# Performance work log

Measured on AMD Instinct MI355X. Metric: run time of the kernel, lower is better.

The kernel has to match this reference:

```python
import jax, jax.numpy as jnp
import numpy as np
from jax import lax

D_MODEL = 512
INPUT_DIM = 64
D_INNER = 1024      # expand * d_model
D_STATE = 128
NHEADS = 16         # d_inner // headdim (headdim = ssm_state//num_heads = 64)
HEADDIM = 64
D_CONV = 4
CONV_DIM = D_INNER + 2 * D_STATE          # 1280 (ngroups=1)
D_IN_PROJ = 2 * D_INNER + 2 * D_STATE + NHEADS  # 2320
BATCH = 2
SEQ = 1024
MASK_RATIO = 0.75
EPS = 1e-5


def setup_inputs() -> dict:
    key = jax.random.key(0)
    ks = jax.random.split(key, 14)
    s = lambda fan: 1.0 / np.sqrt(fan)
    return {
        "x": jax.random.normal(ks[0], (BATCH, SEQ, INPUT_DIM), jnp.float32),
        "conv_emb_w": jax.random.normal(ks[1], (D_MODEL, INPUT_DIM, 3), jnp.float32) * s(INPUT_DIM * 3),
        "conv_emb_b": jax.random.normal(ks[2], (D_MODEL,), jnp.float32) * 0.02,
        "cls_token": jax.random.normal(ks[3], (1, 1, D_MODEL), jnp.float32) * 0.02,
        "in_proj_w": jax.random.normal(ks[4], (D_IN_PROJ, D_MODEL), jnp.float32) * s(D_MODEL),
        "conv1d_w": jax.random.normal(ks[5], (CONV_DIM, 1, D_CONV), jnp.float32) * s(D_CONV),
        "conv1d_b": jax.random.normal(ks[6], (CONV_DIM,), jnp.float32) * 0.02,
        "dt_bias": jax.random.uniform(ks[7], (NHEADS,), jnp.float32, -4.0, 0.0),
        "A_log": jnp.log(jax.random.uniform(ks[8], (NHEADS,), jnp.float32, 1.0, 16.0)),
        "D": jax.random.normal(ks[9], (NHEADS,), jnp.float32),
        "rms_w": jnp.ones((D_INNER,), jnp.float32),
        "out_proj_w": jax.random.normal(ks[10], (D_MODEL, D_INNER), jnp.float32) * s(D_INNER),
        "ln_g": jnp.ones((D_MODEL,), jnp.float32),
        "ln_b": jnp.zeros((D_MODEL,), jnp.float32),
    }


def _forward(x, conv_emb_w, conv_emb_b, cls_token, in_proj_w, conv1d_w, conv1d_b,
             dt_bias, A_log, D, rms_w, out_proj_w, ln_g, ln_b):
    b = x.shape[0]
    # ---- conv embedding: Conv1d(k=3, pad=1) over time ----
    xe = lax.conv_general_dilated(x.transpose(0, 2, 1), conv_emb_w, (1,), [(1, 1)],
                                  dimension_numbers=("NCH", "OIH", "NCH"))
    xe = (xe + conv_emb_b[None, :, None]).transpose(0, 2, 1)  # (b, L, d_model)
    # ---- append CLS token at end ----
    h = jnp.concatenate([xe, jnp.broadcast_to(cls_token, (b, 1, D_MODEL))], axis=1)
    L = h.shape[1]
    # ---- Mamba2 block ----
    zxbcdt = jnp.einsum("bld,ed->ble", h, in_proj_w)  # (b, L, 2320)
    z = zxbcdt[..., :D_INNER]
    xBC = zxbcdt[..., D_INNER:D_INNER + CONV_DIM]
    dt = jax.nn.softplus(zxbcdt[..., -NHEADS:] + dt_bias)  # (b, L, h)
    # causal depthwise conv (pad left d_conv-1) + SiLU
    xBC = lax.conv_general_dilated(xBC.transpose(0, 2, 1), conv1d_w, (1,), [(D_CONV - 1, 0)],
                                   dimension_numbers=("NCH", "OIH", "NCH"),
                                   feature_group_count=CONV_DIM)
    xBC = jax.nn.silu((xBC + conv1d_b[None, :, None]).transpose(0, 2, 1))  # (b, L, 1280)
    x_in = xBC[..., :D_INNER].reshape(b, L, NHEADS, HEADDIM)   # (b, L, h, p)
    B = xBC[..., D_INNER:D_INNER + D_STATE]                     # (b, L, n)
    C = xBC[..., D_INNER + D_STATE:]                            # (b, L, n)
    A = -jnp.exp(A_log)                                         # (h,)
    dA = jnp.exp(dt * A)                                        # (b, L, h)
    # selective state-space scan; state (b, h, p, n)
    def step(state, inp):
        x_t, dt_t, B_t, C_t, dA_t = inp  # (b,h,p) (b,h) (b,n) (b,n) (b,h)
        state = state * dA_t[:, :, None, None] + \
            (dt_t[:, :, None] * x_t)[..., None] * B_t[:, None, None, :]
        y_t = jnp.einsum("bhpn,bn->bhp", state, C_t)
        return state, y_t
    s0 = jnp.zeros((b, NHEADS, HEADDIM, D_STATE), x.dtype)
    _, ys = lax.scan(step, s0, (x_in.transpose(1, 0, 2, 3), dt.transpose(1, 0, 2),
                                B.transpose(1, 0, 2), C.transpose(1, 0, 2),
                                dA.transpose(1, 0, 2)))
    y = ys.transpose(1, 0, 2, 3) + D[None, None, :, None] * x_in  # (b, L, h, p)
    y = y.reshape(b, L, D_INNER)
    # gated RMSNorm: gate first, then normalize
    y = y * jax.nn.silu(z)
    y = y * lax.rsqrt(jnp.mean(y * y, axis=-1, keepdims=True) + EPS) * rms_w
    out = jnp.einsum("ble,de->bld", y, out_proj_w)  # (b, L, d_model)
    # ---- LayerNorm ----
    mu = jnp.mean(out, axis=-1, keepdims=True)
    var = jnp.mean((out - mu) ** 2, axis=-1, keepdims=True)
    out = (out - mu) * lax.rsqrt(var + EPS) * ln_g + ln_b
    return out


def reference(x, conv_emb_w, conv_emb_b, cls_token, in_proj_w, conv1d_w, conv1d_b,
              dt_bias, A_log, D, rms_w, out_proj_w, ln_g, ln_b):
    out = _forward(x, conv_emb_w, conv_emb_b, cls_token, in_proj_w, conv1d_w, conv1d_b,
                   dt_bias, A_log, D, rms_w, out_proj_w, ln_g, ln_b)
    b = out.shape[0]
    cls = out[:, -1:, :]
    body = out[:, :-1, :]                      # (b, SEQ, d)
    len_keep = int(SEQ * (1 - MASK_RATIO))     # 256
    noise = jax.random.uniform(jax.random.fold_in(jax.random.key(0), 1), (b, SEQ))
    ids_shuffle = jnp.argsort(noise, axis=1)
    ids_restore = jnp.argsort(ids_shuffle, axis=1)
    ids_keep = ids_shuffle[:, :len_keep]
    x_masked = jnp.take_along_axis(body, ids_keep[:, :, None], axis=1)
    mask = jnp.where(jnp.arange(SEQ)[None, :] < len_keep, 0.0, 1.0)
    mask = jnp.take_along_axis(jnp.broadcast_to(mask, (b, SEQ)), ids_restore, axis=1)
    x_out = jnp.concatenate([x_masked, cls], axis=1)  # (b, len_keep+1, d)
    return (x_out, mask, ids_restore, ids_keep)
```

## Files before the change

### kernel.cpp

```cpp
#include <hip/hip_runtime.h>
#include <hip/hip_bf16.h>
#include <stdint.h>

#define LTOK  1025
#define NROWS 2050
#define DM    512
#define DIN   1024
#define DST   128
#define NHEAD 16
#define HDIM  64
#define CDIM  1280
#define EPROJ 2320
#define QC    64
#define NCH   17

#define O_RIDX   0
#define O_CB     1024
#define O_CLS    1536
#define O_C1B    2048
#define O_DTB    3328
#define O_ALOG   3344
#define O_DV     3360
#define O_RMSW   3376
#define O_LNG    4400
#define O_LNB    4912
#define O_CW     5440
#define O_IPW    103744
#define O_OPW    1291584
#define O_C1W    1815872
#define O_CX     1820992
#define O_ZX     1952064
#define O_XBC    6708064
#define O_DT     9332064
#define O_LGA    9364864
#define O_Y      9397664
#define O_H      9397664
#define O_X3     10447264
#define O_OUTG   11496864
#define O_SL     11760032
#define O_CLA    16216480
#define O_SL2    16251296
#define O_KEEP   18479520

#define OO_MASK 263168
#define OO_IDR  265216
#define OO_IDK  267264

typedef __attribute__((ext_vector_type(8))) short short8;
typedef __attribute__((ext_vector_type(4))) short shortx4;
typedef __attribute__((ext_vector_type(4))) float floatx4;

__device__ __forceinline__ short f2bs(float f) {
  union { float f; uint32_t u; } v; v.f = f;
  uint32_t r = (v.u + 0x7FFFu + ((v.u >> 16) & 1u)) >> 16;
  return (short)r;
}
__device__ __forceinline__ float bf2f(uint16_t u) {
  return __uint_as_float(((uint32_t)u) << 16);
}

struct InPtrs { const void* p[14]; };

__device__ __forceinline__ uint32_t rotl32(uint32_t v, int d) {
  return (v << d) | (v >> (32 - d));
}
__device__ void threefry2x32(uint32_t k0, uint32_t k1, uint32_t c0, uint32_t c1,
                             uint32_t& o0, uint32_t& o1) {
  uint32_t ks0 = k0, ks1 = k1, ks2 = 0x1BD11BDAu ^ k0 ^ k1;
  uint32_t x0 = c0 + ks0, x1 = c1 + ks1;
#define TF_R4(a,b,c,d) \
  x0 += x1; x1 = rotl32(x1,a); x1 ^= x0; \
  x0 += x1; x1 = rotl32(x1,b); x1 ^= x0; \
  x0 += x1; x1 = rotl32(x1,c); x1 ^= x0; \
  x0 += x1; x1 = rotl32(x1,d); x1 ^= x0;
  TF_R4(13,15,26,6)  x0 += ks1; x1 += ks2 + 1u;
  TF_R4(17,29,16,24) x0 += ks2; x1 += ks0 + 2u;
  TF_R4(13,15,26,6)  x0 += ks0; x1 += ks1 + 3u;
  TF_R4(17,29,16,24) x0 += ks1; x1 += ks2 + 4u;
  TF_R4(13,15,26,6)  x0 += ks2; x1 += ks0 + 5u;
#undef TF_R4
  o0 = x0; o1 = x1;
}

__device__ int detect_is_f32(const uint32_t* w, int nelem) {
  int nw = nelem / 2; if (nw > 16) nw = 16;
  int insane = 0, lozero = 0, anynz = 0;
  for (int i = 0; i < nw; ++i) {
    uint32_t word = w[i];
    if (word != 0u) anynz = 1;
    uint32_t lo = word & 0xffffu;
    if (lo == 0u) { lozero++; continue; }
    float v = __uint_as_float(lo << 16);
    float a = fabsf(v);
    if (!(a >= 1e-8f && a <= 1e4f)) insane++;
  }
  if (insane >= 2) return 1;
  if (lozero == nw && anynz) return 1;
  return 0;
}

__global__ __launch_bounds__(256) void k_convert(InPtrs ptrs, float* ws,
                                                 float* out, int* rowidx) {
  static const int sizes[13] = {98304, 512, 512, 1187840, 5120, 1280,
                                16, 16, 16, 1024, 524288, 512, 512};
  static const int offs[13]  = {O_CW, O_CB, O_CLS, O_IPW, O_C1W, O_C1B,
                                O_DTB, O_ALOG, O_DV, O_RMSW, O_OPW, O_LNG, O_LNB};
  static const int isbf[13]  = {1,0,0,1,0,0,0,0,0,0,1,0,0};
  int t = blockIdx.y;
  int tid = threadIdx.x;

  if (t >= 14) {
    int b = t - 14;
    int idx = blockIdx.x;
    if (idx > 1024) return;
    if (idx == 1024) {
      const uint32_t* cp = (const uint32_t*)ptrs.p[3];
      __shared__ int cf;
      if (tid == 0) cf = detect_is_f32(cp, 512);
      __syncthreads();
      uint16_t* hout = (uint16_t*)(ws + O_H);
      for (int cch = tid; cch < DM; cch += 256) {
        float v = cf ? ((const float*)cp)[cch] : bf2f(((const uint16_t*)cp)[cch]);
        hout[((long)(b * LTOK + 1024)) * DM + cch] = (uint16_t)f2bs(v);
      }
      return;
    }
    const uint32_t* xp = (const uint32_t*)ptrs.p[0];
    __shared__ int xf;
    if (tid == 0) xf = detect_is_f32(xp, 131072);
    __syncthreads();
    if (tid < 192) {
      int i = tid / 3, k = tid % 3;
      int tt = idx + k - 1;
      float v = 0.f;
      if (tt >= 0 && tt < 1024) {
        long src = ((long)(b * 1024 + tt)) * 64 + i;
        v = xf ? ((const float*)xp)[src] : bf2f(((const uint16_t*)xp)[src]);
      }
      ((uint16_t*)(ws + O_X3))[((long)(b * 1024 + idx)) * 192 + tid] = (uint16_t)f2bs(v);
    }
    return;
  }

  if (t == 13) {
    int bx = blockIdx.x;
    if (bx < 257) {
      int base = (bx * 256 + tid) * 4;
      if (base < 263168)
        *(float4*)(ws + O_OUTG + base) = make_float4(0.f, 0.f, 0.f, 0.f);
      return;
    }
    if (bx < 512 || bx >= 544) return;
    int rb = bx - 512;
    int seg = rb & 15, b = rb >> 4;
    uint8_t* keep = (uint8_t*)(ws + O_KEEP);
    __shared__ float vals[1024];
    uint32_t fk0, fk1;
    threefry2x32(0u, 0u, 0u, 1u, fk0, fk1);
#pragma unroll
    for (int k = 0; k < 4; ++k) {
      int i = tid + k * 256;
      uint32_t o0, o1;
      threefry2x32(fk0, fk1, 0u, (uint32_t)(b * 1024 + i), o0, o1);
      uint32_t bits = o0 ^ o1;
      vals[i] = __uint_as_float((bits >> 9) | 0x3f800000u) - 1.0f;
    }
    __syncthreads();
    int tg = seg * 64 + (tid >> 2);
    int qq = tid & 3;
    float v = vals[tg];
    int r = 0;
    int j0 = qq * 256;
    for (int it = 0; it < 256; ++it) {
      int j = j0 + ((it + qq * 8) & 255);
      float vj = vals[j];
      r += (vj < v || (vj == v && j < tg)) ? 1 : 0;
    }
    r += __shfl_xor(r, 1, 64);
    r += __shfl_xor(r, 2, 64);
    if (qq == 0) {
      out[OO_IDR + b * 1024 + tg] = (float)r;
      out[OO_MASK + b * 1024 + tg] = (r < 256) ? 0.0f : 1.0f;
      keep[b * LTOK + tg] = (r < 256) ? 1 : 0;
      if (r < 256) {
        out[OO_IDK + b * 256 + r] = (float)tg;
        rowidx[b * 257 + r] = b * LTOK + tg;
      }
      if (tg == 0) {
        rowidx[b * 257 + 256] = b * LTOK + 1024;
        keep[b * LTOK + 1024] = 1;
      }
    }
    return;
  }

  int n = sizes[t];
  const uint32_t* w = (const uint32_t*)ptrs.p[t + 1];
  __shared__ int sf;
  if (tid == 0) sf = detect_is_f32(w, n);
  __syncthreads();
  int base = (blockIdx.x * 256 + tid) * 4;
  if (base >= n) return;
  if (isbf[t]) {
    ushort4 o;
    if (sf) {
      const float4 vv = *(const float4*)((const float*)w + base);
      o.x = (uint16_t)f2bs(vv.x); o.y = (uint16_t)f2bs(vv.y);
      o.z = (uint16_t)f2bs(vv.z); o.w = (uint16_t)f2bs(vv.w);
    } else {
      const uint32_t* s = w + (base >> 1);
      uint32_t w0 = s[0], w1 = s[1];
      o.x = (uint16_t)(w0 & 0xffffu); o.y = (uint16_t)(w0 >> 16);
      o.z = (uint16_t)(w1 & 0xffffu); o.w = (uint16_t)(w1 >> 16);
    }
    *(ushort4*)((uint16_t*)(ws + offs[t]) + base) = o;
  } else {
    float* dst = ws + offs[t];
    if (sf) {
      *(float4*)(dst + base) = *(const float4*)((const float*)w + base);
    } else {
      const uint32_t* s = w + (base >> 1);
      uint32_t w0 = s[0], w1 = s[1];
      float4 o;
      o.x = __uint_as_float((w0 & 0xffffu) << 16);
      o.y = __uint_as_float(w0 & 0xffff0000u);
      o.z = __uint_as_float((w1 & 0xffffu) << 16);
      o.w = __uint_as_float(w1 & 0xffff0000u);
      *(float4*)(dst + base) = o;
    }
  }
}

__global__ __launch_bounds__(256) void k_bgemm(
    const void* __restrict__ A, const uint16_t* __restrict__ Bw,
    void* __restrict__ C, const float* __restrict__ bias,
    const int* __restrict__ rowmap, int M, int N, int K, int ldc,
    int cmode, int abf, int obf) {
  __shared__ __align__(16) short sA[2][128 * 40];
  __shared__ __align__(16) short sB[2][128 * 40];
  int tid = threadIdx.x;
  int lane = tid & 63, w = tid >> 6;
  int lm = lane & 15, q = lane >> 4;
  int wm = (w >> 1) * 64, wn = (w & 1) * 64;
  int bm = blockIdx.y * 128, bn = blockIdx.x * 128;
  int gz = gridDim.z;
  int Ks = K / gz;
  int kbase = blockIdx.z * Ks;
  int nk = Ks >> 5;

  int srow[4], scol[4];
  long aoff[4]; bool aok[4]; long boff[4]; bool bok[4];
#pragma unroll
  for (int it = 0; it < 4; ++it) {
    int e4 = (tid + it * 256) * 4;
    srow[it] = e4 >> 5; scol[it] = e4 & 31;
    int gm = bm + srow[it];
    aok[it] = gm < M;
    aoff[it] = aok[it] ? (long)(rowmap ? rowmap[gm] : gm) * K : 0;
    int gn = bn + srow[it];
    bok[it] = gn < N;
    boff[it] = bok[it] ? (long)gn * K : 0;
  }

  auto gload = [&](int kt, float4* vaf, ushort4* vau, ushort4* vb) {
    int kc = kbase + kt * 32;
#pragma unroll
    for (int it = 0; it < 4; ++it) {
      if (abf) {
        if (aok[it]) vau[it] = *(const ushort4*)((const uint16_t*)A + aoff[it] + kc + scol[it]);
        else { vau[it].x = 0; vau[it].y = 0; vau[it].z = 0; vau[it].w = 0; }
      } else {
        vaf[it] = aok[it] ? *(const float4*)((const float*)A + aoff[it] + kc + scol[it])
                          : make_float4(0.f, 0.f, 0.f, 0.f);
      }
      if (bok[it]) vb[it] = *(const ushort4*)(Bw + boff[it] + kc + scol[it]);
      else { vb[it].x = 0; vb[it].y = 0; vb[it].z = 0; vb[it].w = 0; }
    }
  };
  auto sstore = [&](int buf, const float4* vaf, const ushort4* vau, const ushort4* vb) {
#pragma unroll
    for (int it = 0; it < 4; ++it) {
      if (abf)
        *(ushort4*)&sA[buf][srow[it] * 40 + scol[it]] = vau[it];
      else
        *(shortx4*)&sA[buf][srow[it] * 40 + scol[it]] =
            shortx4{f2bs(vaf[it].x), f2bs(vaf[it].y), f2bs(vaf[it].z), f2bs(vaf[it].w)};
      *(ushort4*)&sB[buf][srow[it] * 40 + scol[it]] = vb[it];
    }
  };

  floatx4 acc[4][4] = {};
  float4 vaf[4], naf[4];
  ushort4 vau[4], nau[4], vb[4], nb[4];

  gload(0, vaf, vau, vb);
  sstore(0, vaf, vau, vb);
  for (int kt = 0; kt < nk; ++kt) {
    int cur = kt & 1;
    if (kt + 1 < nk) gload(kt + 1, naf, nau, nb);
    __syncthreads();
    short8 afrag[4], bfrag[4];
#pragma unroll
    for (int i = 0; i < 4; ++i)
      afrag[i] = *(const short8*)&sA[cur][(wm + i * 16 + lm) * 40 + q * 8];
#pragma unroll
    for (int j = 0; j < 4; ++j)
      bfrag[j] = *(const short8*)&sB[cur][(wn + j * 16 + lm) * 40 + q * 8];
#pragma unroll
    for (int i = 0; i < 4; ++i)
#pragma unroll
      for (int j = 0; j < 4; ++j)
        acc[i][j] = __builtin_amdgcn_mfma_f32_16x16x32_bf16(afrag[i], bfrag[j], acc[i][j], 0, 0, 0);
    if (kt + 1 < nk) sstore(1 - cur, naf, nau, nb);
  }

#pragma unroll
  for (int i = 0; i < 4; ++i) {
    int rowl = wm + i * 16 + q * 4;
#pragma unroll
    for (int reg = 0; reg < 4; ++reg) {
      int r = bm + rowl + reg;
      if (r >= M) continue;
      long crow = cmode ? (long)((r >> 10) * LTOK + (r & 1023)) : (long)r;
#pragma unroll
      for (int j = 0; j < 4; ++j) {
        int ccol = bn + wn + j * 16 + lm;
        if (ccol < N) {
          float v = acc[i][j][reg];
          if (gz > 1) {
            atomicAdd(&((float*)C)[crow * ldc + ccol], v);
          } else {
            if (bias) v += bias[ccol];
            if (obf) ((uint16_t*)C)[crow * ldc + ccol] = (uint16_t)f2bs(v);
            else ((float*)C)[crow * ldc + ccol] = v;
          }
        }
      }
    }
  }
}

__global__ __launch_bounds__(256) void k_conv1d(const uint16_t* __restrict__ zx,
                                                const float* __restrict__ w,
                                                const float* __restrict__ bias,
                                                uint16_t* __restrict__ xbc,
                                                const float* __restrict__ dtb,
                                                const float* __restrict__ alog,
                                                float* __restrict__ dt,
                                                float* __restrict__ lga) {
  long rp_ = blockIdx.x;
  if (rp_ >= NROWS) {
    int idx = (int)(rp_ - NROWS) * 256 + threadIdx.x;
    if (idx < NROWS * NHEAD) {
      int rr = idx >> 4, h = idx & 15;
      float xv = bf2f(zx[(long)rr * EPROJ + (EPROJ - NHEAD) + h]) + dtb[h];
      float dtv = (xv > 20.f) ? xv : log1pf(expf(xv));
      dt[idx] = dtv;
      lga[idx] = dtv * (-expf(alog[h]));
    }
    return;
  }
  {
    int xcd = (int)(rp_ & 7), slot = (int)(rp_ >> 3);
    rp_ = (xcd < 2) ? (long)xcd * 257 + slot
                    : (long)514 + (long)(xcd - 2) * 256 + slot;
  }
  long r = rp_;
  int b = (int)(r / LTOK), t = (int)(r % LTOK);
  for (int c4 = threadIdx.x * 4; c4 < CDIM; c4 += 1024) {
    float4 bi = *(const float4*)(bias + c4);
    float a0 = bi.x, a1 = bi.y, a2 = bi.z, a3 = bi.w;
    float4 w0 = *(const float4*)(w + (c4 + 0) * 4);
    float4 w1 = *(const float4*)(w + (c4 + 1) * 4);
    float4 w2 = *(const float4*)(w + (c4 + 2) * 4);
    float4 w3 = *(const float4*)(w + (c4 + 3) * 4);
    float wr0[4] = {w0.x, w0.y, w0.z, w0.w};
    float wr1[4] = {w1.x, w1.y, w1.z, w1.w};
    float wr2[4] = {w2.x, w2.y, w2.z, w2.w};
    float wr3[4] = {w3.x, w3.y, w3.z, w3.w};
#pragma unroll
    for (int k = 0; k < 4; ++k) {
      int tt = t - 3 + k;
      if (tt >= 0) {
        ushort4 xv = *(const ushort4*)(zx + ((long)(b * LTOK + tt)) * EPROJ + DIN + c4);
        a0 = fmaf(wr0[k], bf2f(xv.x), a0);
        a1 = fmaf(wr1[k], bf2f(xv.y), a1);
        a2 = fmaf(wr2[k], bf2f(xv.z), a2);
        a3 = fmaf(wr3[k], bf2f(xv.w), a3);
      }
    }
    ushort4 o;
    o.x = (uint16_t)f2bs(a0 / (1.f + expf(-a0)));
    o.y = (uint16_t)f2bs(a1 / (1.f + expf(-a1)));
    o.z = (uint16_t)f2bs(a2 / (1.f + expf(-a2)));
    o.w = (uint16_t)f2bs(a3 / (1.f + expf(-a3)));
    *(ushort4*)(xbc + r * CDIM + c4) = o;
  }
}

__global__ __launch_bounds__(256) void k_ssd1(const uint16_t* __restrict__ xbc,
                                              const float* __restrict__ dt,
                                              const float* __restrict__ lga,
                                              float* __restrict__ SL,
                                              float* __restrict__ CLA) {
  int blk = blockIdx.x;
  int c = blk % NCH;
  int hh = blk / NCH;
  int h = hh & 15, b = hh >> 4;
  int tid = threadIdx.x;
  int lane = tid & 63, w = tid >> 6;
  int lm = lane & 15, q = lane >> 4;

  __shared__ __align__(16) short sBT[128 * 72];
  __shared__ __align__(16) short sXT[64 * 72];
  __shared__ float wwv[64];

  int t0 = c * QC;
  const uint16_t* base = xbc + (long)b * LTOK * CDIM;

  if (tid < 64) {
    int t = t0 + tid;
    float dtv = (t < LTOK) ? dt[((long)(b * LTOK + t)) * NHEAD + h] : 0.f;
    float v   = (t < LTOK) ? lga[((long)(b * LTOK + t)) * NHEAD + h] : 0.f;
#pragma unroll
    for (int off = 1; off < 64; off <<= 1) {
      float u = __shfl_up(v, off, 64);
      if (lane >= off) v += u;
    }
    float clEnd = __shfl(v, 63, 64);
    wwv[tid] = __expf(clEnd - v) * dtv;
    CLA[(long)blk * 64 + tid] = v;
  }
  __syncthreads();

#pragma unroll
  for (int k = 0; k < 8; ++k) {
    int e4 = (tid + k * 256) * 4;
    int row = e4 >> 7, col = e4 & 127;
    int t = t0 + row;
    ushort4 bv = {0,0,0,0};
    if (t < LTOK) bv = *(const ushort4*)(base + (long)t * CDIM + DIN + col);
    float wv = wwv[row];
    sBT[(col  )*72+row]=f2bs(bf2f(bv.x)*wv); sBT[(col+1)*72+row]=f2bs(bf2f(bv.y)*wv);
    sBT[(col+2)*72+row]=f2bs(bf2f(bv.z)*wv); sBT[(col+3)*72+row]=f2bs(bf2f(bv.w)*wv);
  }
#pragma unroll
  for (int k = 0; k < 4; ++k) {
    int e4 = (tid + k * 256) * 4;
    int row = e4 >> 6, col = e4 & 63;
    int t = t0 + row;
    ushort4 xv = {0,0,0,0};
    if (t < LTOK) xv = *(const ushort4*)(base + (long)t * CDIM + h * 64 + col);
    sXT[(col  )*72+row]=(short)xv.x; sXT[(col+1)*72+row]=(short)xv.y;
    sXT[(col+2)*72+row]=(short)xv.z; sXT[(col+3)*72+row]=(short)xv.w;
  }
  __syncthreads();

  floatx4 s[2][4] = {};
#pragma unroll
  for (int kb = 0; kb < 2; ++kb) {
    short8 bfr[4];
#pragma unroll
    for (int ct = 0; ct < 4; ++ct)
      bfr[ct] = *(const short8*)&sXT[(ct*16 + lm)*72 + kb*32 + q*8];
#pragma unroll
    for (int nt = 0; nt < 2; ++nt) {
      short8 a = *(const short8*)&sBT[((w*2+nt)*16 + lm)*72 + kb*32 + q*8];
#pragma unroll
      for (int ct = 0; ct < 4; ++ct)
        s[nt][ct] = __builtin_amdgcn_mfma_f32_16x16x32_bf16(a, bfr[ct], s[nt][ct], 0, 0, 0);
    }
  }
  float* slp = SL + (long)blk * 8192;
#pragma unroll
  for (int nt = 0; nt < 2; ++nt)
#pragma unroll
    for (int ct = 0; ct < 4; ++ct)
#pragma unroll
      for (int reg = 0; reg < 4; ++reg) {
        int n = (w*2+nt)*16 + q*4 + reg;
        int p = ct*16 + lm;
        slp[n*64 + p] = s[nt][ct][reg];
      }
}

__global__ __launch_bounds__(256) void k_comb(const float* __restrict__ SL,
                                              const float* __restrict__ CLA,
                                              uint16_t* __restrict__ SL2) {
  int bx = blockIdx.x;
  int piece = bx & 15;
  int hh = bx >> 4;
  int off = piece * 512 + threadIdx.x * 2;
  long cb0 = (long)hh * NCH;
  float P[NCH];
  float2 tmp[NCH];
#pragma unroll
  for (int c = 0; c < NCH; ++c) {
    P[c] = __expf(CLA[(cb0 + c) * 64 + 63]);
    tmp[c] = *(const float2*)(SL + (cb0 + c) * 8192 + off);
  }
  float2 s = make_float2(0.f, 0.f);
#pragma unroll
  for (int c = 0; c < NCH; ++c) {
    uint32_t packed = (uint32_t)(uint16_t)f2bs(s.x) | ((uint32_t)(uint16_t)f2bs(s.y) << 16);
    *(uint32_t*)(SL2 + (cb0 + c) * 8192 + off) = packed;
    s.x = fmaf(P[c], s.x, tmp[c].x);
    s.y = fmaf(P[c], s.y, tmp[c].y);
  }
}

__global__ __launch_bounds__(256) void k_ssd3(const uint16_t* __restrict__ xbc,
                                              const float* __restrict__ dt,
                                              const uint16_t* __restrict__ SL2,
                                              const float* __restrict__ CLA,
                                              const uint8_t* __restrict__ keepf,
                                              float* __restrict__ Y) {
  int blk = blockIdx.x;
  int c = blk % NCH;
  int hh = blk / NCH;
  int h = hh & 15, b = hh >> 4;
  int tid = threadIdx.x;
  int lane = tid & 63, w = tid >> 6;
  int lm = lane & 15, q = lane >> 4;

  __shared__ __align__(16) short sST[64 * 136];
  __shared__ __align__(16) short sXT[64 * 72];
  __shared__ __align__(16) short sM[64 * 72];
  __shared__ float dtw[64], clA[64], evec[64];
  __shared__ uint8_t kf[64];

  int t0 = c * QC;
  const uint16_t* base = xbc + (long)b * LTOK * CDIM;
  const uint16_t* slp = SL2 + (long)blk * 8192;

  if (tid < 64) {
    int t = t0 + tid;
    dtw[tid] = (t < LTOK) ? dt[((long)(b * LTOK + t)) * NHEAD + h] : 0.f;
    float v = CLA[(long)blk * 64 + tid];
    clA[tid] = v;
    evec[tid] = __expf(v);
    kf[tid] = (t < LTOK) ? keepf[b * LTOK + t] : 0;
  }

#pragma unroll
  for (int k = 0; k < 4; ++k) {
    int e4 = (tid + k * 256) * 4;
    int row = e4 >> 6, col = e4 & 63;
    int t = t0 + row;
    ushort4 xv = {0,0,0,0};
    if (t < LTOK) xv = *(const ushort4*)(base + (long)t * CDIM + h * 64 + col);
    sXT[(col  )*72+row]=(short)xv.x; sXT[(col+1)*72+row]=(short)xv.y;
    sXT[(col+2)*72+row]=(short)xv.z; sXT[(col+3)*72+row]=(short)xv.w;
  }
#pragma unroll
  for (int k = 0; k < 8; ++k) {
    int e4 = (tid + k * 256) * 4;
    int n = e4 >> 6, p = e4 & 63;
    ushort4 sv = *(const ushort4*)(slp + n * 64 + p);
    sST[(p  )*136+n]=(short)sv.x; sST[(p+1)*136+n]=(short)sv.y;
    sST[(p+2)*136+n]=(short)sv.z; sST[(p+3)*136+n]=(short)sv.w;
  }
  __syncthreads();

  short8 cfr[4];
  int tA = t0 + w*16 + lm;
  bool tAok = tA < LTOK;
#pragma unroll
  for (int kb = 0; kb < 4; ++kb) {
    short8 z = {0,0,0,0,0,0,0,0};
    cfr[kb] = tAok ? *(const short8*)(base + (long)tA * CDIM + DIN + DST + kb*32 + q*8) : z;
  }

  floatx4 g[4] = {};
#pragma unroll
  for (int kb = 0; kb < 4; ++kb) {
#pragma unroll
    for (int ct = 0; ct < 4; ++ct) {
      int tB = t0 + ct*16 + lm;
      short8 z = {0,0,0,0,0,0,0,0};
      short8 bb = (tB < LTOK) ? *(const short8*)(base + (long)tB * CDIM + DIN + kb*32 + q*8) : z;
      g[ct] = __builtin_amdgcn_mfma_f32_16x16x32_bf16(cfr[kb], bb, g[ct], 0, 0, 0);
    }
  }
#pragma unroll
  for (int ct = 0; ct < 4; ++ct) {
    int tp = ct*16 + lm;
#pragma unroll
    for (int reg = 0; reg < 4; ++reg) {
      int tl = w*16 + q*4 + reg;
      float m = 0.f;
      if (tp <= tl) m = g[ct][reg] * __expf(clA[tl] - clA[tp]) * dtw[tp];
      sM[tl*72 + tp] = f2bs(m);
    }
  }
  floatx4 y2[4] = {};
#pragma unroll
  for (int kb = 0; kb < 4; ++kb) {
#pragma unroll
    for (int ct = 0; ct < 4; ++ct) {
      short8 bb = *(const short8*)&sST[(ct*16 + lm)*136 + kb*32 + q*8];
      y2[ct] = __builtin_amdgcn_mfma_f32_16x16x32_bf16(cfr[kb], bb, y2[ct], 0, 0, 0);
    }
  }
  __syncthreads();
  floatx4 y1[4] = {};
#pragma unroll
  for (int kb = 0; kb < 2; ++kb) {
    short8 a = *(const short8*)&sM[(w*16 + lm)*72 + kb*32 + q*8];
#pragma unroll
    for (int ct = 0; ct < 4; ++ct) {
      short8 bb = *(const short8*)&sXT[(ct*16 + lm)*72 + kb*32 + q*8];
      y1[ct] = __builtin_amdgcn_mfma_f32_16x16x32_bf16(a, bb, y1[ct], 0, 0, 0);
    }
  }
#pragma unroll
  for (int reg = 0; reg < 4; ++reg) {
    int tl = w*16 + q*4 + reg;
    int t = t0 + tl;
    if (t < LTOK && kf[tl]) {
      float ev = evec[tl];
#pragma unroll
      for (int ct = 0; ct < 4; ++ct) {
        int p = ct*16 + lm;
        Y[((long)(b * LTOK + t)) * DIN + h * 64 + p] = y1[ct][reg] + ev * y2[ct][reg];
      }
    }
  }
}

__global__ __launch_bounds__(256) void k_gaterms(const float* __restrict__ Y,
                                                 const uint16_t* __restrict__ xbc,
                                                 const uint16_t* __restrict__ zx,
                                                 const float* __restrict__ Dv,
                                                 const float* __restrict__ rmsw,
                                                 const int* __restrict__ ridx,
                                                 uint16_t* __restrict__ G) {
  int rr = blockIdx.x;
  long r = ridx[rr];
  int tid = threadIdx.x;
  int e = tid * 4;
  int h = tid >> 4;
  float4 a = *(const float4*)(Y + r * DIN + e);
  const ushort4 xu = *(const ushort4*)(xbc + r * CDIM + e);
  const ushort4 zu = *(const ushort4*)(zx + r * EPROJ + e);
  float Dh = Dv[h];
  float y0 = a.x + Dh * bf2f(xu.x), y1 = a.y + Dh * bf2f(xu.y);
  float y2 = a.z + Dh * bf2f(xu.z), y3 = a.w + Dh * bf2f(xu.w);
  float z0 = bf2f(zu.x), z1 = bf2f(zu.y), z2 = bf2f(zu.z), z3 = bf2f(zu.w);
  float g0 = y0 * (z0 / (1.f + expf(-z0)));
  float g1 = y1 * (z1 / (1.f + expf(-z1)));
  float g2 = y2 * (z2 / (1.f + expf(-z2)));
  float g3 = y3 * (z3 / (1.f + expf(-z3)));
  __shared__ float red[256];
  red[tid] = g0*g0 + g1*g1 + g2*g2 + g3*g3;
  __syncthreads();
  for (int st = 128; st; st >>= 1) {
    if (tid < st) red[tid] += red[tid + st];
    __syncthreads();
  }
  float scale = rsqrtf(red[0] * (1.0f / 1024.0f) + 1e-5f);
  float4 rw = *(const float4*)(rmsw + e);
  ushort4 o;
  o.x = (uint16_t)f2bs(g0 * scale * rw.x);
  o.y = (uint16_t)f2bs(g1 * scale * rw.y);
  o.z = (uint16_t)f2bs(g2 * scale * rw.z);
  o.w = (uint16_t)f2bs(g3 * scale * rw.w);
  *(ushort4*)(G + (long)rr * DIN + e) = o;
}

__global__ __launch_bounds__(256) void k_ln(const float* __restrict__ outg,
                                            const float* __restrict__ lng,
                                            const float* __restrict__ lnb,
                                            float* __restrict__ out) {
  int r = blockIdx.x;
  int tid = threadIdx.x;
  const float2 v = *(const float2*)(outg + (long)r * DM + tid * 2);
  __shared__ float red[256];
  red[tid] = v.x + v.y;
  __syncthreads();
  for (int st = 128; st; st >>= 1) { if (tid < st) red[tid] += red[tid + st]; __syncthreads(); }
  float mu = red[0] * (1.0f / 512.0f);
  __syncthreads();
  float dx = v.x - mu, dy = v.y - mu;
  red[tid] = dx * dx + dy * dy;
  __syncthreads();
  for (int st = 128; st; st >>= 1) { if (tid < st) red[tid] += red[tid + st]; __syncthreads(); }
  float sc = rsqrtf(red[0] * (1.0f / 512.0f) + 1e-5f);
  int c = tid * 2;
  out[(long)r * DM + c]     = dx * sc * lng[c] + lnb[c];
  out[(long)r * DM + c + 1] = dy * sc * lng[c + 1] + lnb[c + 1];
}

extern "C" void kernel_launch(void* const* d_in, const int* in_sizes, int n_in,
                              void* d_out, int out_size, void* d_ws, size_t ws_size,
                              hipStream_t stream) {
  float* ws = (float*)d_ws;
  float* out = (float*)d_out;
  int* rowidx = (int*)(ws + O_RIDX);
  InPtrs ip;
  for (int i = 0; i < 14; ++i) ip.p[i] = d_in[i];

  hipLaunchKernelGGL(k_convert, dim3(1160, 16), dim3(256), 0, stream, ip, ws, out, rowidx);
  hipLaunchKernelGGL(k_bgemm, dim3(4, 16, 1), dim3(256), 0, stream,
                     (const void*)(ws + O_X3), (const uint16_t*)(ws + O_CW),
                     (void*)(ws + O_H), ws + O_CB, (const int*)nullptr,
                     2048, 512, 192, 512, 1, 1, 1);
  hipLaunchKernelGGL(k_bgemm, dim3(19, 17, 1), dim3(256), 0, stream,
                     (const void*)(ws + O_H), (const uint16_t*)(ws + O_IPW),
                     (void*)(ws + O_ZX), (const float*)nullptr, (const int*)nullptr,
                     2050, 2320, 512, 2320, 0, 1, 1);
  hipLaunchKernelGGL(k_conv1d, dim3(2179), dim3(256), 0, stream,
                     (const uint16_t*)(ws + O_ZX), ws + O_C1W, ws + O_C1B,
                     (uint16_t*)(ws + O_XBC),
                     ws + O_DTB, ws + O_ALOG, ws + O_DT, ws + O_LGA);
  hipLaunchKernelGGL(k_ssd1, dim3(32 * NCH), dim3(256), 0, stream,
                     (const uint16_t*)(ws + O_XBC), ws + O_DT, ws + O_LGA,
                     ws + O_SL, ws + O_CLA);
  hipLaunchKernelGGL(k_comb, dim3(512), dim3(256), 0, stream,
                     ws + O_SL, ws + O_CLA, (uint16_t*)(ws + O_SL2));
  hipLaunchKernelGGL(k_ssd3, dim3(32 * NCH), dim3(256), 0, stream,
                     (const uint16_t*)(ws + O_XBC), ws + O_DT,
                     (const uint16_t*)(ws + O_SL2), ws + O_CLA,
                     (const uint8_t*)(ws + O_KEEP), ws + O_Y);
  hipLaunchKernelGGL(k_gaterms, dim3(514), dim3(256), 0, stream,
                     ws + O_Y, (const uint16_t*)(ws + O_XBC),
                     (const uint16_t*)(ws + O_ZX), ws + O_DV, ws + O_RMSW,
                     (const int*)rowidx, (uint16_t*)(ws + O_X3));
  hipLaunchKernelGGL(k_bgemm, dim3(4, 5, 4), dim3(256), 0, stream,
                     (const void*)(ws + O_X3), (const uint16_t*)(ws + O_OPW),
                     (void*)(ws + O_OUTG), (const float*)nullptr, (const int*)nullptr,
                     514, 512, 1024, 512, 0, 1, 0);
  hipLaunchKernelGGL(k_ln, dim3(514), dim3(256), 0, stream,
                     ws + O_OUTG, ws + O_LNG, ws + O_LNB, out);
}
```

Baseline: 218.3 us.

## Add specialized 64x64 MFMA GEMMs for conv-embed and out-proj with split-K partials

Replaces the generic 128x128 bgemm for the conv-embedding GEMM (K=192) and the out-projection GEMM with dedicated 64x64-tile kernels. Each loads its full K slice into LDS once and runs 16x16x32 bf16 MFMAs, which gives more blocks for these small problems. The out-projection now writes four split-K partial buffers instead of atomically accumulating into a zeroed buffer. The LayerNorm kernel sums those partials, so the zeroing pass in the convert kernel is removed. The cost is extra workspace and four reads per element in LayerNorm.

```diff
diff --git a/kernel.cpp b/kernel.cpp
--- a/kernel.cpp
+++ b/kernel.cpp
@@ -41,12 +41,14 @@
 #define O_CLA    16216480
 #define O_SL2    16251296
 #define O_KEEP   18479520
+#define O_OUTP   18480128
 
 #define OO_MASK 263168
 #define OO_IDR  265216
 #define OO_IDK  267264
 
 typedef __attribute__((ext_vector_type(8))) short short8;
+typedef __attribute__((ext_vector_type(8))) unsigned short ushortx8;
 typedef __attribute__((ext_vector_type(4))) short shortx4;
 typedef __attribute__((ext_vector_type(4))) float floatx4;
 
@@ -144,12 +146,6 @@
 
   if (t == 13) {
     int bx = blockIdx.x;
-    if (bx < 257) {
-      int base = (bx * 256 + tid) * 4;
-      if (base < 263168)
-        *(float4*)(ws + O_OUTG + base) = make_float4(0.f, 0.f, 0.f, 0.f);
-      return;
-    }
     if (bx < 512 || bx >= 544) return;
     int rb = bx - 512;
     int seg = rb & 15, b = rb >> 4;
@@ -227,6 +223,96 @@
       o.z = __uint_as_float((w1 & 0xffffu) << 16);
       o.w = __uint_as_float(w1 & 0xffff0000u);
       *(float4*)(dst + base) = o;
+    }
+  }
+}
+
+__global__ __launch_bounds__(256) void k_cgemm(const uint16_t* __restrict__ A,
+                                               const uint16_t* __restrict__ Bw,
+                                               uint16_t* __restrict__ H,
+                                               const float* __restrict__ bias) {
+  __shared__ __align__(16) short sA[64 * 200];
+  __shared__ __align__(16) short sB[64 * 200];
+  int tid = threadIdx.x;
+  int lane = tid & 63, w = tid >> 6;
+  int lm = lane & 15, q = lane >> 4;
+  int bm = blockIdx.y * 64, bn = blockIdx.x * 64;
+
+#pragma unroll
+  for (int it = 0; it < 6; ++it) {
+    int li = it * 256 + tid;
+    int row = li / 24, col = (li % 24) * 8;
+    ushortx8 av = *(const ushortx8*)(A + (long)(bm + row) * 192 + col);
+    *(ushortx8*)&sA[row * 200 + col] = av;
+    ushortx8 bv = *(const ushortx8*)(Bw + (long)(bn + row) * 192 + col);
+    *(ushortx8*)&sB[row * 200 + col] = bv;
+  }
+  __syncthreads();
+
+  floatx4 acc[4] = {};
+#pragma unroll
+  for (int kb = 0; kb < 6; ++kb) {
+    short8 a = *(const short8*)&sA[(w * 16 + lm) * 200 + kb * 32 + q * 8];
+#pragma unroll
+    for (int ct = 0; ct < 4; ++ct) {
+      short8 b = *(const short8*)&sB[(ct * 16 + lm) * 200 + kb * 32 + q * 8];
+      acc[ct] = __builtin_amdgcn_mfma_f32_16x16x32_bf16(a, b, acc[ct], 0, 0, 0);
+    }
+  }
+#pragma unroll
+  for (int reg = 0; reg < 4; ++reg) {
+    int r = bm + w * 16 + q * 4 + reg;
+    long crow = (long)((r >> 10) * LTOK + (r & 1023));
+#pragma unroll
+    for (int ct = 0; ct < 4; ++ct) {
+      int cc = bn + ct * 16 + lm;
+      H[crow * DM + cc] = (uint16_t)f2bs(acc[ct][reg] + bias[cc]);
+    }
+  }
+}
+
+__global__ __launch_bounds__(256) void k_ogemm(const uint16_t* __restrict__ A,
+                                               const uint16_t* __restrict__ Bw,
+                                               float* __restrict__ OUTP) {
+  __shared__ __align__(16) short sA[64 * 264];
+  __shared__ __align__(16) short sB[64 * 264];
+  int tid = threadIdx.x;
+  int lane = tid & 63, w = tid >> 6;
+  int lm = lane & 15, q = lane >> 4;
+  int bm = blockIdx.y * 64, bn = blockIdx.x * 64;
+  int kbase = blockIdx.z * 256;
+
+#pragma unroll
+  for (int it = 0; it < 8; ++it) {
+    int li = it * 256 + tid;
+    int row = li >> 5, col = (li & 31) * 8;
+    int gm = bm + row;
+    ushortx8 av = {0,0,0,0,0,0,0,0};
+    if (gm < 514) av = *(const ushortx8*)(A + (long)gm * 1024 + kbase + col);
+    *(ushortx8*)&sA[row * 264 + col] = av;
+    ushortx8 bv = *(const ushortx8*)(Bw + (long)(bn + row) * 1024 + kbase + col);
+    *(ushortx8*)&sB[row * 264 + col] = bv;
+  }
+  __syncthreads();
+
+  floatx4 acc[4] = {};
+#pragma unroll
+  for (int kb = 0; kb < 8; ++kb) {
+    short8 a = *(const short8*)&sA[(w * 16 + lm) * 264 + kb * 32 + q * 8];
+#pragma unroll
+    for (int ct = 0; ct < 4; ++ct) {
+      short8 b = *(const short8*)&sB[(ct * 16 + lm) * 264 + kb * 32 + q * 8];
+      acc[ct] = __builtin_amdgcn_mfma_f32_16x16x32_bf16(a, b, acc[ct], 0, 0, 0);
+    }
+  }
+  float* op = OUTP + (long)blockIdx.z * 263168;
+#pragma unroll
+  for (int reg = 0; reg < 4; ++reg) {
+    int r = bm + w * 16 + q * 4 + reg;
+    if (r < 514) {
+#pragma unroll
+      for (int ct = 0; ct < 4; ++ct)
+        op[(long)r * 512 + bn + ct * 16 + lm] = acc[ct][reg];
     }
   }
 }
@@ -668,13 +754,20 @@
   *(ushort4*)(G + (long)rr * DIN + e) = o;
 }
 
-__global__ __launch_bounds__(256) void k_ln(const float* __restrict__ outg,
+__global__ __launch_bounds__(256) void k_ln(const float* __restrict__ outp,
                                             const float* __restrict__ lng,
                                             const float* __restrict__ lnb,
                                             float* __restrict__ out) {
   int r = blockIdx.x;
   int tid = threadIdx.x;
-  const float2 v = *(const float2*)(outg + (long)r * DM + tid * 2);
+  long e = (long)r * DM + tid * 2;
+  float2 v0 = *(const float2*)(outp + e);
+  float2 v1 = *(const float2*)(outp + 263168 + e);
+  float2 v2 = *(const float2*)(outp + 2 * 263168 + e);
+  float2 v3 = *(const float2*)(outp + 3 * 263168 + e);
+  float2 v;
+  v.x = ((v0.x + v1.x) + v2.x) + v3.x;
+  v.y = ((v0.y + v1.y) + v2.y) + v3.y;
   __shared__ float red[256];
   red[tid] = v.x + v.y;
   __syncthreads();
@@ -701,10 +794,9 @@
   for (int i = 0; i < 14; ++i) ip.p[i] = d_in[i];
 
   hipLaunchKernelGGL(k_convert, dim3(1160, 16), dim3(256), 0, stream, ip, ws, out, rowidx);
-  hipLaunchKernelGGL(k_bgemm, dim3(4, 16, 1), dim3(256), 0, stream,
-                     (const void*)(ws + O_X3), (const uint16_t*)(ws + O_CW),
-                     (void*)(ws + O_H), ws + O_CB, (const int*)nullptr,
-                     2048, 512, 192, 512, 1, 1, 1);
+  hipLaunchKernelGGL(k_cgemm, dim3(8, 32), dim3(256), 0, stream,
+                     (const uint16_t*)(ws + O_X3), (const uint16_t*)(ws + O_CW),
+                     (uint16_t*)(ws + O_H), ws + O_CB);
   hipLaunchKernelGGL(k_bgemm, dim3(19, 17, 1), dim3(256), 0, stream,
                      (const void*)(ws + O_H), (const uint16_t*)(ws + O_IPW),
                      (void*)(ws + O_ZX), (const float*)nullptr, (const int*)nullptr,
@@ -726,10 +818,9 @@
                      ws + O_Y, (const uint16_t*)(ws + O_XBC),
                      (const uint16_t*)(ws + O_ZX), ws + O_DV, ws + O_RMSW,
                      (const int*)rowidx, (uint16_t*)(ws + O_X3));
-  hipLaunchKernelGGL(k_bgemm, dim3(4, 5, 4), dim3(256), 0, stream,
-                     (const void*)(ws + O_X3), (const uint16_t*)(ws + O_OPW),
-                     (void*)(ws + O_OUTG), (const float*)nullptr, (const int*)nullptr,
-                     514, 512, 1024, 512, 0, 1, 0);
+  hipLaunchKernelGGL(k_ogemm, dim3(8, 9, 4), dim3(256), 0, stream,
+                     (const uint16_t*)(ws + O_X3), (const uint16_t*)(ws + O_OPW),
+                     ws + O_OUTP);
   hipLaunchKernelGGL(k_ln, dim3(514), dim3(256), 0, stream,
-                     ws + O_OUTG, ws + O_LNG, ws + O_LNB, out);
-}
+                     ws + O_OUTP, ws + O_LNG, ws + O_LNB, out);
+}
```

New measurement: 199.9 us. 8.4% less time.
